# Optimization experiments

Hardware: AMD Instinct MI355X
Metric: run time of the kernel (lower is better)

The kernel has to match this reference:

```python
import jax, jax.numpy as jnp
import numpy as np

DEPTH = 2   # depth
H = 8       # heads
DH = 32     # dim_head
DIM = 256   # model dim (= H*DH)
W = 2       # sliding_window_size
C = 4       # compress_block_size == selection_block_size
NSEL = 2    # num_selected_blocks
B, S = 4, 2048


def layernorm(x, g, b, eps=1e-5):
    m = x.mean(-1, keepdims=True)
    v = jnp.var(x, axis=-1, keepdims=True)
    return (x - m) * jax.lax.rsqrt(v + eps) * g + b


def msoftmax(s, mask):
    # numerically-safe masked softmax; rows with no visible key output zeros
    s = jnp.where(mask, s, -1e9)
    p = jax.nn.softmax(s, axis=-1)
    return jnp.where(jnp.any(mask, axis=-1, keepdims=True), p, 0.0)


def nsa(x, Wq, Wk, Wv, Wg, Wo):
    # Native sparse attention: compressed + top-k selected blocks + sliding window,
    # combined with per-head sigmoid gates.
    b, s, d = x.shape
    nb = s // C
    q = (x @ Wq).reshape(b, s, H, DH).transpose(0, 2, 1, 3)  # [B,H,S,DH]
    k = (x @ Wk).reshape(b, s, H, DH).transpose(0, 2, 1, 3)
    v = (x @ Wv).reshape(b, s, H, DH).transpose(0, 2, 1, 3)
    scale = DH ** -0.5
    t = jnp.arange(s)

    # ---- compressed branch: mean-pooled KV blocks, causal over fully-past blocks
    kb = k.reshape(b, H, nb, C, DH)
    vb = v.reshape(b, H, nb, C, DH)
    kc = kb.mean(3)
    vc = vb.mean(3)
    sc = jnp.einsum('bhsd,bhnd->bhsn', q, kc) * scale       # [B,H,S,nb]
    blk_end = jnp.arange(nb) * C + (C - 1)
    cmask = blk_end[None, :] <= t[:, None]                   # [S,nb]
    pc = msoftmax(sc, cmask[None, None])
    oc = jnp.einsum('bhsn,bhnd->bhsd', pc, vc)

    # ---- selection branch: own block always + top (NSEL-1) blocks by compressed score
    own = t // C                                             # [S]
    not_own = jnp.arange(nb)[None, :] != own[:, None]        # [S,nb]
    sel_scores = jnp.where(not_own[None, None], pc, -1.0)
    top_idx = jax.lax.top_k(sel_scores, NSEL - 1)[1]         # [B,H,S,NSEL-1]
    own_idx = jnp.broadcast_to(own[None, None, :, None], (b, H, s, 1))
    idx = jnp.concatenate([own_idx, top_idx], axis=-1)       # [B,H,S,NSEL]
    idxf = idx.reshape(b, H, s * NSEL, 1, 1)
    sk = jnp.take_along_axis(kb, idxf, axis=2).reshape(b, H, s, NSEL * C, DH)
    sv = jnp.take_along_axis(vb, idxf, axis=2).reshape(b, H, s, NSEL * C, DH)
    pos = (idx[..., None] * C + jnp.arange(C)).reshape(b, H, s, NSEL * C)
    fmask = pos <= t[None, None, :, None]
    sf = jnp.einsum('bhsd,bhskd->bhsk', q, sk) * scale
    pf = msoftmax(sf, fmask)
    of = jnp.einsum('bhsk,bhskd->bhsd', pf, sv)

    # ---- sliding-window branch: causal local window of W tokens (incl. self)
    off = jnp.arange(W) - (W - 1)
    wpos = t[:, None] + off[None, :]                         # [S,W]
    widx = jnp.clip(wpos, 0, s - 1)
    kw = jnp.take(k, widx.reshape(-1), axis=2).reshape(b, H, s, W, DH)
    vw = jnp.take(v, widx.reshape(-1), axis=2).reshape(b, H, s, W, DH)
    sw = jnp.einsum('bhsd,bhsjd->bhsj', q, kw) * scale
    pw = msoftmax(sw, (wpos >= 0)[None, None])
    ow = jnp.einsum('bhsj,bhsjd->bhsd', pw, vw)

    # ---- gated combine + output projection
    g = jax.nn.sigmoid(x @ Wg).reshape(b, s, 3, H).transpose(0, 3, 1, 2)  # [B,H,S,3]
    o = g[..., 0:1] * oc + g[..., 1:2] * of + g[..., 2:3] * ow
    return o.transpose(0, 2, 1, 3).reshape(b, s, H * DH) @ Wo


def forward(x, ln_a_g, ln_a_b, Wq, Wk, Wv, Wg, Wo, ln_f_g, ln_f_b, W1, b1, W2, b2):
    for l in range(DEPTH):
        for j in range(2):  # two attention sub-layers per block
            i = l * 2 + j
            h = layernorm(x, ln_a_g[i], ln_a_b[i])
            x = x + nsa(h, Wq[i], Wk[i], Wv[i], Wg[i], Wo[i])
        h = layernorm(x, ln_f_g[l], ln_f_b[l])
        h = h @ W1[l] + b1[l]
        h = jnp.where(h > 0, h, 0.01 * h)  # LeakyReLU
        x = x + h @ W2[l] + b2[l]
    return x


def setup_inputs() -> dict:
    key = jax.random.key(0)
    ks = jax.random.split(key, 8)
    A = DEPTH * 2
    r = lambda k, shp: jax.random.normal(k, shp, jnp.float32) * 0.02
    return {
        'x': jax.random.normal(ks[0], (B, S, DIM), jnp.float32),
        'ln_a_g': jnp.ones((A, DIM), jnp.float32),
        'ln_a_b': jnp.zeros((A, DIM), jnp.float32),
        'Wq': r(ks[1], (A, DIM, H * DH)),
        'Wk': r(ks[2], (A, DIM, H * DH)),
        'Wv': r(ks[3], (A, DIM, H * DH)),
        'Wg': r(ks[4], (A, DIM, 3 * H)),
        'Wo': r(ks[5], (A, H * DH, DIM)),
        'ln_f_g': jnp.ones((DEPTH, DIM), jnp.float32),
        'ln_f_b': jnp.zeros((DEPTH, DIM), jnp.float32),
        'W1': r(ks[6], (DEPTH, DIM, 2 * DIM)),
        'b1': jnp.zeros((DEPTH, 2 * DIM), jnp.float32),
        'W2': r(ks[7], (DEPTH, 2 * DIM, DIM)),
        'b2': jnp.zeros((DEPTH, DIM), jnp.float32),
    }


def reference(x, ln_a_g, ln_a_b, Wq, Wk, Wv, Wg, Wo, ln_f_g, ln_f_b, W1, b1, W2, b2):
    return forward(x, ln_a_g, ln_a_b, Wq, Wk, Wv, Wg, Wo, ln_f_g, ln_f_b, W1, b1, W2, b2)
```

## Files before the change

kernel.cpp:

```cpp
#include <hip/hip_runtime.h>
#include <hip/hip_bf16.h>
#include <math.h>

#define NH 8
#define DH 32
#define DIM 256
#define SEQ 2048
#define BATCH 4
#define NB 512
#define QKS 512
#define VGS 320
#define SCALE 0.17677669529663687f

typedef short short8v __attribute__((ext_vector_type(8)));
typedef float float4v __attribute__((ext_vector_type(4)));

__device__ __forceinline__ float sigmoidf_(float x){ return 1.f/(1.f+__expf(-x)); }
__device__ __forceinline__ ushort f2bf(float f){
  uint b = __float_as_uint(f);
  return (ushort)((b + 0x7fffu + ((b>>16)&1u)) >> 16);
}
__device__ __forceinline__ float bf2f(ushort u){ return __uint_as_float(((uint)u)<<16); }
__device__ __forceinline__ float bflo(uint u){ return __uint_as_float(u<<16); }
__device__ __forceinline__ float bfhi(uint u){ return __uint_as_float(u & 0xffff0000u); }
__device__ __forceinline__ uint pk2(float a, float b){ return (uint)f2bf(a) | ((uint)f2bf(b)<<16); }
__device__ __forceinline__ void bfu4_to_f32(uint4 u, float* f){
  f[0]=bflo(u.x); f[1]=bfhi(u.x);
  f[2]=bflo(u.y); f[3]=bfhi(u.y);
  f[4]=bflo(u.z); f[5]=bfhi(u.z);
  f[6]=bflo(u.w); f[7]=bfhi(u.w);
}
__device__ __forceinline__ void bfu2_to_f32(uint2 u, float* f){
  f[0]=bflo(u.x); f[1]=bfhi(u.x);
  f[2]=bflo(u.y); f[3]=bfhi(u.y);
}

__global__ void copy_f32(const float* __restrict__ in, float* __restrict__ out, int n4){
  int i = blockIdx.x*blockDim.x + threadIdx.x;
  if (i < n4) ((float4*)out)[i] = ((const float4*)in)[i];
}

__global__ void build_wqk(const float* __restrict__ Wq, const float* __restrict__ Wk, float* __restrict__ out){
  int i = blockIdx.x*256 + threadIdx.x;
  if (i >= 4*256*QKS) return;
  int col = i & 511, rk = (i>>9)&255, l = i>>17;
  out[i] = (col < 256) ? Wq[((size_t)l*256+rk)*256+col] : Wk[((size_t)l*256+rk)*256+col-256];
}
__global__ void build_wvgT(const float* __restrict__ Wv, const float* __restrict__ Wg, ushort* __restrict__ out){
  int i = blockIdx.x*256 + threadIdx.x;
  if (i >= 4*VGS*256) return;
  int k = i & 255, n = (i>>8)%VGS, l = i/(VGS*256);
  float v = 0.f;
  if      (n < 256) v = Wv[((size_t)l*256+k)*256+n];
  else if (n < 280) v = Wg[((size_t)l*256+k)*24 + (n-256)];
  out[i] = f2bf(v);
}
__global__ void build_wT(const float* __restrict__ in, ushort* __restrict__ out, int L, int K, int N){
  int i = blockIdx.x*256 + threadIdx.x;
  if (i >= L*K*N) return;
  int k = i % K, n = (i/K) % N, l = i/(K*N);
  out[i] = f2bf(in[((size_t)l*K+k)*N+n]);
}

__global__ __launch_bounds__(256) void ln_k(const float* __restrict__ x, const float* __restrict__ g,
                                            const float* __restrict__ b, float* __restrict__ h,
                                            ushort* __restrict__ hb){
  int row  = blockIdx.x*4 + (threadIdx.x>>6);
  int lane = threadIdx.x & 63;
  int c = lane*4;
  const float* xr = x + (size_t)row*DIM + c;
  float4 v = *(const float4*)xr;
  float s = v.x+v.y+v.z+v.w;
  float q = v.x*v.x+v.y*v.y+v.z*v.z+v.w*v.w;
  #pragma unroll
  for (int off=32; off>0; off>>=1){ s += __shfl_xor(s, off); q += __shfl_xor(q, off); }
  float mean = s * (1.f/DIM);
  float var  = q * (1.f/DIM) - mean*mean;
  float rs = rsqrtf(var + 1e-5f);
  float4 gg = *(const float4*)(g + c);
  float4 bb = *(const float4*)(b + c);
  float4 o;
  o.x = (v.x-mean)*rs*gg.x + bb.x;
  o.y = (v.y-mean)*rs*gg.y + bb.y;
  o.z = (v.z-mean)*rs*gg.z + bb.z;
  o.w = (v.w-mean)*rs*gg.w + bb.w;
  *(float4*)(h + (size_t)row*DIM + c) = o;
  uint2 u;
  u.x = pk2(o.x, o.y);
  u.y = pk2(o.z, o.w);
  *(uint2*)&hb[(size_t)row*DIM + c] = u;
}

template<bool BIAS, bool LEAKY, bool ACC>
__global__ __launch_bounds__(256) void gemm_f32(const float* __restrict__ A, const float* __restrict__ B,
                                                const float* __restrict__ bias, float* __restrict__ C,
                                                int M, int N, int K){
  __shared__ float As[32][132];
  __shared__ float Bs[32][68];
  int tid = threadIdx.x;
  int m0 = blockIdx.x*128, n0 = blockIdx.y*64;
  int tx = tid & 15, ty = tid >> 4;
  int ar = tid >> 1;
  int ac = (tid & 1)*16;
  int bk = tid >> 3;
  int bn = (tid & 7)*8;
  const float* Ap = A + (size_t)(m0+ar)*K + ac;
  const float* Bp = B + (size_t)bk*N + n0 + bn;
  float4 apre[4], bpre[2];
  #pragma unroll
  for (int j=0;j<4;j++) apre[j] = *(const float4*)(Ap + 4*j);
  bpre[0] = *(const float4*)Bp;
  bpre[1] = *(const float4*)(Bp + 4);
  float acc[8][4];
  #pragma unroll
  for (int i=0;i<8;i++)
    #pragma unroll
    for (int j=0;j<4;j++) acc[i][j]=0.f;
  for (int k0=0; k0<K; k0+=32){
    #pragma unroll
    for (int j=0;j<4;j++){
      As[ac+4*j+0][ar]=apre[j].x; As[ac+4*j+1][ar]=apre[j].y;
      As[ac+4*j+2][ar]=apre[j].z; As[ac+4*j+3][ar]=apre[j].w;
    }
    *(float4*)&Bs[bk][bn]   = bpre[0];
    *(float4*)&Bs[bk][bn+4] = bpre[1];
    __syncthreads();
    if (k0 + 32 < K){
      #pragma unroll
      for (int j=0;j<4;j++) apre[j] = *(const float4*)(Ap + k0 + 32 + 4*j);
      bpre[0] = *(const float4*)(Bp + (size_t)(k0+32)*N);
      bpre[1] = *(const float4*)(Bp + (size_t)(k0+32)*N + 4);
    }
    #pragma unroll
    for (int kk=0;kk<32;kk++){
      float4 bv  = *(const float4*)&Bs[kk][tx*4];
      float4 av0 = *(const float4*)&As[kk][ty*8];
      float4 av1 = *(const float4*)&As[kk][ty*8+4];
      float av[8] = {av0.x,av0.y,av0.z,av0.w,av1.x,av1.y,av1.z,av1.w};
      float bw[4] = {bv.x,bv.y,bv.z,bv.w};
      #pragma unroll
      for (int i=0;i<8;i++)
        #pragma unroll
        for (int j=0;j<4;j++) acc[i][j] += av[i]*bw[j];
    }
    __syncthreads();
  }
  #pragma unroll
  for (int i=0;i<8;i++){
    int m = m0 + ty*8 + i;
    #pragma unroll
    for (int j=0;j<4;j++){
      int n = n0 + tx*4 + j;
      float val = acc[i][j];
      if (BIAS)  val += bias[n];
      if (LEAKY) val = val > 0.f ? val : 0.01f*val;
      float* cp = C + (size_t)m*N + n;
      if (ACC) val += *cp;
      *cp = val;
    }
  }
}

template<bool BIAS, bool LEAKY, bool ACC, bool OBF16>
__global__ __launch_bounds__(256) void gemm_bf16(const ushort* __restrict__ A, const ushort* __restrict__ Bt,
                                                 const float* __restrict__ bias, void* __restrict__ Cv,
                                                 int M, int N, int K){
  __shared__ ushort Al[128*64];
  __shared__ ushort Bl[64*64];
  int tid = threadIdx.x;
  int m0 = blockIdx.x*128, n0 = blockIdx.y*64;
  int w = tid>>6, lane = tid&63;
  int wm = w>>1, wn = w&1;
  float4v acc[4][2];
  #pragma unroll
  for (int i=0;i<4;i++)
    #pragma unroll
    for (int j=0;j<2;j++) acc[i][j] = (float4v){0.f,0.f,0.f,0.f};
  for (int k0=0; k0<K; k0+=64){
    #pragma unroll
    for (int i=0;i<4;i++){
      int id = tid + 256*i;
      int r = id>>3, c = id&7;
      *(uint4*)&Al[r*64 + ((c ^ (r&7))*8)] = *(const uint4*)&A[(size_t)(m0+r)*K + k0 + c*8];
    }
    #pragma unroll
    for (int i=0;i<2;i++){
      int id = tid + 256*i;
      int r = id>>3, c = id&7;
      *(uint4*)&Bl[r*64 + ((c ^ (r&7))*8)] = *(const uint4*)&Bt[(size_t)(n0+r)*K + k0 + c*8];
    }
    __syncthreads();
    #pragma unroll
    for (int kk=0; kk<2; ++kk){
      short8v a[4], bfr[2];
      #pragma unroll
      for (int mf=0; mf<4; mf++){
        int r = wm*64 + mf*16 + (lane&15);
        int c = (kk*4 + (lane>>4)) ^ (r&7);
        a[mf] = *(short8v*)&Al[r*64 + c*8];
      }
      #pragma unroll
      for (int nf=0; nf<2; nf++){
        int r = wn*32 + nf*16 + (lane&15);
        int c = (kk*4 + (lane>>4)) ^ (r&7);
        bfr[nf] = *(short8v*)&Bl[r*64 + c*8];
      }
      #pragma unroll
      for (int mf=0; mf<4; mf++)
        #pragma unroll
        for (int nf=0; nf<2; nf++)
          acc[mf][nf] = __builtin_amdgcn_mfma_f32_16x16x32_bf16(a[mf], bfr[nf], acc[mf][nf], 0, 0, 0);
    }
    __syncthreads();
  }
  #pragma unroll
  for (int nf=0; nf<2; nf++){
    int col = n0 + wn*32 + nf*16 + (lane&15);
    float bv = BIAS ? bias[col] : 0.f;
    #pragma unroll
    for (int mf=0; mf<4; mf++){
      #pragma unroll
      for (int r=0; r<4; r++){
        int row = m0 + wm*64 + mf*16 + (lane>>4)*4 + r;
        float vv = acc[mf][nf][r];
        if (BIAS) vv += bv;
        if (LEAKY) vv = vv > 0.f ? vv : 0.01f*vv;
        if (OBF16) ((ushort*)Cv)[(size_t)row*N + col] = f2bf(vv);
        else {
          float* C = (float*)Cv;
          if (ACC) vv += C[(size_t)row*N + col];
          C[(size_t)row*N + col] = vv;
        }
      }
    }
  }
}

__global__ void pool_k(const float* __restrict__ qk, const ushort* __restrict__ vg,
                       float* __restrict__ kc, ushort* __restrict__ vct){
  int i = blockIdx.x*256 + threadIdx.x;
  if (i >= BATCH*NH*NB*DH) return;
  int d = i & 31, n = (i >> 5) & 511, h = (i >> 14) & 7, b = i >> 17;
  size_t kb = ((size_t)(b*SEQ + n*4))*QKS + 256 + h*DH + d;
  kc[i] = 0.25f*(qk[kb] + qk[kb+QKS] + qk[kb+2*QKS] + qk[kb+3*QKS]);
  size_t vb = ((size_t)(b*SEQ + n*4))*VGS + h*DH + d;
  float pv = 0.25f*(bf2f(vg[vb]) + bf2f(vg[vb+VGS]) + bf2f(vg[vb+2*VGS]) + bf2f(vg[vb+3*VGS]));
  vct[(((size_t)(b*NH + h))*DH + d)*NB + n] = f2bf(pv);
}

__global__ __launch_bounds__(512, 4) void nsa_attn(
    const float* __restrict__ qk, const ushort* __restrict__ vg,
    const float* __restrict__ kc, const ushort* __restrict__ vct,
    ushort* __restrict__ o)
{
  __shared__ float  kt[64*32];
  __shared__ ushort vcT[32*72];
  __shared__ ushort Pl[64*72];
  __shared__ float4 meta[8*64];
  int e = blockIdx.x;
  int hh = e & 7;
  int b  = (e >> 3) & 3;
  int qq = (e >> 5) & 7;
  int r  = e >> 8;
  int g  = (r==0) ? (31-qq) : (r==1) ? qq : (r==2) ? (23-qq) : (8+qq);
  int tid = threadIdx.x;
  int w = tid >> 6, lane = tid & 63;
  const float*  kcg  = kc  + ((size_t)(b*NH + hh)*NB)*DH;
  const ushort* vctg = vct + ((size_t)(b*NH + hh)*DH)*NB;

  float4v acc0 = (float4v){0.f,0.f,0.f,0.f};
  float4v acc1 = (float4v){0.f,0.f,0.f,0.f};

  {
    int t = g*64 + lane;
    int own = t >> 2, nvis = (t+1) >> 2;
    int nmax = 16*(g+1);
    float qv[32];
    {
      const float4* qr = (const float4*)(qk + ((size_t)b*SEQ + t)*QKS + hh*DH);
      #pragma unroll
      for (int d8=0; d8<8; d8++){
        float4 a4 = qr[d8];
        qv[4*d8]=a4.x; qv[4*d8+1]=a4.y; qv[4*d8+2]=a4.z; qv[4*d8+3]=a4.w;
      }
    }
    float l = 0.f, best = -1e30f;
    int bn1 = -1;

    int tiles = (g + 4) >> 2;
    for (int ti=0; ti<tiles; ++ti){
      int base = ti*64;
      if (ti) __syncthreads();
      {
        const float4* sk = (const float4*)(kcg + (size_t)base*DH);
        ((float4*)kt)[tid] = sk[tid];
        if (tid < 256){
          int sd = tid >> 3, sn = (tid & 7)*8;
          *(uint4*)&vcT[sd*72 + sn] = *(const uint4*)&vctg[(size_t)sd*NB + base + sn];
        }
      }
      __syncthreads();
      int jm = nmax - base - 8*w;
      jm = jm < 0 ? 0 : (jm > 8 ? 8 : jm);
      float ps[8];
      #pragma unroll
      for (int j=0;j<8;j++) ps[j]=0.f;
      for (int j=0; j<jm; ++j){
        int rr = 8*w + j;
        int n = base + rr;
        const float4* kp = (const float4*)&kt[rr*32];
        float s = 0.f;
        #pragma unroll
        for (int d8=0; d8<8; d8++){
          float4 k4 = kp[d8];
          s += qv[4*d8]*k4.x + qv[4*d8+1]*k4.y + qv[4*d8+2]*k4.z + qv[4*d8+3]*k4.w;
        }
        s *= SCALE;
        bool act = (n < nvis);
        if (act && n != own && s > best){ best = s; bn1 = n; }
        float p = act ? __expf(s) : 0.f;
        l += p;
        ps[j] = p;
      }
      {
        uint4 u0;
        u0.x = pk2(ps[0],ps[1]);  u0.y = pk2(ps[2],ps[3]);
        u0.z = pk2(ps[4],ps[5]);  u0.w = pk2(ps[6],ps[7]);
        *(uint4*)&Pl[lane*72 + w*8] = u0;
      }
      __syncthreads();
      if (w < 4){
        #pragma unroll
        for (int ks=0; ks<2; ++ks){
          short8v bfrag = *(short8v*)&Pl [(16*w + (lane&15))*72 + ks*32 + (lane>>4)*8];
          short8v a0    = *(short8v*)&vcT[(lane&15)*72          + ks*32 + (lane>>4)*8];
          short8v a1    = *(short8v*)&vcT[((lane&15)+16)*72     + ks*32 + (lane>>4)*8];
          acc0 = __builtin_amdgcn_mfma_f32_16x16x32_bf16(a0, bfrag, acc0, 0, 0, 0);
          acc1 = __builtin_amdgcn_mfma_f32_16x16x32_bf16(a1, bfrag, acc1, 0, 0, 0);
        }
      }
    }
    meta[w*64 + lane] = make_float4(l, best, __int_as_float(bn1), 0.f);
  }
  __syncthreads();

  if (w < 4){
    int c = lane & 15, m = lane >> 4;
    int tokidx = w*16 + c;
    int t = g*64 + tokidx;
    int own = t >> 2, nvis = (t+1) >> 2;
    int dA = 4*m, dB = 16 + 4*m;
    float q8[8];
    {
      const float* qrow = qk + ((size_t)b*SEQ + t)*QKS + hh*DH;
      float4 a4 = *(const float4*)(qrow + dA);
      float4 b4 = *(const float4*)(qrow + dB);
      q8[0]=a4.x; q8[1]=a4.y; q8[2]=a4.z; q8[3]=a4.w;
      q8[4]=b4.x; q8[5]=b4.y; q8[6]=b4.z; q8[7]=b4.w;
    }
    float out8[8];
    #pragma unroll
    for (int j=0;j<4;j++){ out8[j] = acc0[j]; out8[4+j] = acc1[j]; }
    float ll = 0.f, bb = -1e30f;
    int bn = (own==0) ? 1 : 0;
    #pragma unroll
    for (int sp=0; sp<8; ++sp){
      float4 m4 = meta[sp*64 + tokidx];
      ll += m4.x;
      int mi = __float_as_int(m4.z);
      if (m4.y > bb || (m4.y == bb && mi >= 0 && mi < bn)){ bb = m4.y; bn = mi; }
    }
    const ushort* gr = vg + ((size_t)b*SEQ + t)*VGS + 256;
    float g0 = sigmoidf_(bf2f(gr[hh])), g1 = sigmoidf_(bf2f(gr[8+hh])), g2 = sigmoidf_(bf2f(gr[16+hh]));
    float inv = (nvis > 0) ? g0/ll : 0.f;
    #pragma unroll
    for (int j=0;j<8;j++) out8[j] *= inv;

    const float*  kb2 = qk + (size_t)b*SEQ*QKS + 256 + hh*DH;
    const ushort* vb2 = vg + (size_t)b*SEQ*VGS + hh*DH;
    float s2[8];
    float m2 = -1e30f;
    #pragma unroll
    for (int ki=0; ki<8; ++ki){
      int tt = (ki<4 ? own : bn)*4 + (ki&3);
      float s = -1e30f;
      if (tt <= t){
        const float* kr = kb2 + (size_t)tt*QKS;
        float4 a4 = *(const float4*)(kr + dA);
        float4 c4 = *(const float4*)(kr + dB);
        float ps = q8[0]*a4.x + q8[1]*a4.y + q8[2]*a4.z + q8[3]*a4.w
                 + q8[4]*c4.x + q8[5]*c4.y + q8[6]*c4.z + q8[7]*c4.w;
        ps += __shfl_xor(ps, 16);
        ps += __shfl_xor(ps, 32);
        s = ps*SCALE;
        m2 = fmaxf(m2, s);
      }
      s2[ki] = s;
    }
    float l2 = 0.f;
    #pragma unroll
    for (int ki=0; ki<8; ++ki)
      if (s2[ki] > -1e29f) l2 += __expf(s2[ki] - m2);
    float inv2 = g1/l2;
    #pragma unroll
    for (int ki=0; ki<8; ++ki){
      int tt = (ki<4 ? own : bn)*4 + (ki&3);
      if (tt <= t){
        float pw = __expf(s2[ki] - m2) * inv2;
        float fA[4], fB[4];
        bfu2_to_f32(*(const uint2*)(vb2 + (size_t)tt*VGS + dA), fA);
        bfu2_to_f32(*(const uint2*)(vb2 + (size_t)tt*VGS + dB), fB);
        #pragma unroll
        for (int j=0;j<4;j++){ out8[j] += pw*fA[j]; out8[4+j] += pw*fB[j]; }
      }
    }

    int tp = (t>0) ? t-1 : 0;
    float sa, sb;
    {
      const float* ka = kb2 + (size_t)tp*QKS;
      const float* kb4= kb2 + (size_t)t *QKS;
      float4 a0 = *(const float4*)(ka + dA), a1 = *(const float4*)(ka + dB);
      float4 b0 = *(const float4*)(kb4 + dA), b1 = *(const float4*)(kb4 + dB);
      float pa_ = q8[0]*a0.x + q8[1]*a0.y + q8[2]*a0.z + q8[3]*a0.w
                + q8[4]*a1.x + q8[5]*a1.y + q8[6]*a1.z + q8[7]*a1.w;
      float pb_ = q8[0]*b0.x + q8[1]*b0.y + q8[2]*b0.z + q8[3]*b0.w
                + q8[4]*b1.x + q8[5]*b1.y + q8[6]*b1.z + q8[7]*b1.w;
      pa_ += __shfl_xor(pa_, 16); pa_ += __shfl_xor(pa_, 32);
      pb_ += __shfl_xor(pb_, 16); pb_ += __shfl_xor(pb_, 32);
      sa = pa_*SCALE; sb = pb_*SCALE;
    }
    float m3 = (t>0) ? fmaxf(sa, sb) : sb;
    float pa = (t>0) ? __expf(sa-m3) : 0.f;
    float pb = __expf(sb-m3);
    float inv3 = g2/(pa+pb);
    float va[4], vaB[4], vbv[4], vbB[4];
    bfu2_to_f32(*(const uint2*)(vb2 + (size_t)tp*VGS + dA), va);
    bfu2_to_f32(*(const uint2*)(vb2 + (size_t)tp*VGS + dB), vaB);
    bfu2_to_f32(*(const uint2*)(vb2 + (size_t)t *VGS + dA), vbv);
    bfu2_to_f32(*(const uint2*)(vb2 + (size_t)t *VGS + dB), vbB);
    ushort* orow = o + ((size_t)b*SEQ + t)*DIM + hh*DH;
    float rrA[4], rrB[4];
    #pragma unroll
    for (int j=0;j<4;j++){
      rrA[j] = out8[j]   + (pa*va[j]  + pb*vbv[j])*inv3;
      rrB[j] = out8[4+j] + (pa*vaB[j] + pb*vbB[j])*inv3;
    }
    uint2 uA, uB;
    uA.x = pk2(rrA[0], rrA[1]); uA.y = pk2(rrA[2], rrA[3]);
    uB.x = pk2(rrB[0], rrB[1]); uB.y = pk2(rrB[2], rrB[3]);
    *(uint2*)&orow[dA] = uA;
    *(uint2*)&orow[dB] = uB;
  }
}

extern "C" void kernel_launch(void* const* d_in, const int* in_sizes, int n_in,
                              void* d_out, int out_size, void* d_ws, size_t ws_size,
                              hipStream_t stream) {
  const float* x_in   = (const float*)d_in[0];
  const float* ln_a_g = (const float*)d_in[1];
  const float* ln_a_b = (const float*)d_in[2];
  const float* Wq     = (const float*)d_in[3];
  const float* Wk     = (const float*)d_in[4];
  const float* Wv     = (const float*)d_in[5];
  const float* Wg     = (const float*)d_in[6];
  const float* Wo     = (const float*)d_in[7];
  const float* ln_f_g = (const float*)d_in[8];
  const float* ln_f_b = (const float*)d_in[9];
  const float* W1     = (const float*)d_in[10];
  const float* b1     = (const float*)d_in[11];
  const float* W2     = (const float*)d_in[12];
  const float* b2     = (const float*)d_in[13];

  float* xout = (float*)d_out;
  float* ws = (float*)d_ws;
  const size_t NTOK = (size_t)BATCH*SEQ;
  float* h    = ws;
  float* qkb  = h    + NTOK*DIM;
  float* kcb  = qkb  + NTOK*QKS;
  ushort* vctb = (ushort*)(kcb + (size_t)BATCH*NH*NB*DH);
  float* wqk  = (float*)(vctb + (size_t)BATCH*NH*NB*DH);
  ushort* hb   = (ushort*)(wqk + (size_t)4*DIM*QKS);
  ushort* vgu  = hb   + NTOK*DIM;
  ushort* obu  = vgu  + NTOK*VGS;
  ushort* midu = obu  + NTOK*DIM;
  ushort* wvgT = midu + NTOK*512;
  ushort* woT  = wvgT + (size_t)4*VGS*DIM;
  ushort* w1T  = woT  + (size_t)4*DIM*DIM;
  ushort* w2T  = w1T  + (size_t)2*512*DIM;

  copy_f32<<<2048, 256, 0, stream>>>(x_in, xout, (int)(NTOK*DIM/4));
  build_wqk <<<(4*256*QKS+255)/256, 256, 0, stream>>>(Wq, Wk, wqk);
  build_wvgT<<<(4*VGS*256+255)/256, 256, 0, stream>>>(Wv, Wg, wvgT);
  build_wT  <<<(4*256*256+255)/256, 256, 0, stream>>>(Wo, woT, 4, 256, 256);
  build_wT  <<<(2*256*512+255)/256, 256, 0, stream>>>(W1, w1T, 2, 256, 512);
  build_wT  <<<(2*512*256+255)/256, 256, 0, stream>>>(W2, w2T, 2, 512, 256);

  dim3 gqk(64,8), gvg(64,5), g4(64,4), g8(64,8);
  for (int i=0;i<4;i++){
    ln_k<<<2048,256,0,stream>>>(xout, ln_a_g + i*DIM, ln_a_b + i*DIM, h, hb);
    gemm_f32<false,false,false><<<gqk,256,0,stream>>>(h, wqk + (size_t)i*DIM*QKS, nullptr, qkb, 8192,QKS,256);
    gemm_bf16<false,false,false,true><<<gvg,256,0,stream>>>(hb, wvgT + (size_t)i*VGS*DIM, nullptr, vgu, 8192,VGS,256);
    pool_k<<<2048,256,0,stream>>>(qkb, vgu, kcb, vctb);
    nsa_attn<<<1024,512,0,stream>>>(qkb, vgu, kcb, vctb, obu);
    gemm_bf16<false,false,true,false><<<g4,256,0,stream>>>(obu, woT + (size_t)i*DIM*DIM, nullptr, xout, 8192,DIM,256);
    if (i & 1){
      int l = i >> 1;
      ln_k<<<2048,256,0,stream>>>(xout, ln_f_g + l*DIM, ln_f_b + l*DIM, h, hb);
      gemm_bf16<true,true,false,true><<<g8,256,0,stream>>>(hb,   w1T + (size_t)l*512*DIM, b1 + l*512, midu, 8192,512,256);
      gemm_bf16<true,false,true,false><<<g4,256,0,stream>>>(midu, w2T + (size_t)l*DIM*512, b2 + l*DIM, xout, 8192,DIM,512);
    }
  }
}
```

Measured before the change: 597.2 us.

## Process 128 queries per attention block with 4 waves for compressed-K reuse

The NSA attention kernel now handles 128 query tokens per block with 256 threads instead of 64 tokens with 512 threads. Each thread scores two queries against two compressed keys per step, and each wave issues four MFMAs per k-step, so every compressed-key tile loaded into shared memory serves twice as many queries. The aim is to cut redundant compressed-KV loads and the idle waves in the MFMA and epilogue phases. The cost is higher register pressure, fewer blocks (512), and a simpler causal load-balancing order that may leave the longest blocks unevenly spread across CUs.

```diff
diff --git a/kernel.cpp b/kernel.cpp
--- a/kernel.cpp
+++ b/kernel.cpp
@@ -24,12 +24,6 @@
 __device__ __forceinline__ float bflo(uint u){ return __uint_as_float(u<<16); }
 __device__ __forceinline__ float bfhi(uint u){ return __uint_as_float(u & 0xffff0000u); }
 __device__ __forceinline__ uint pk2(float a, float b){ return (uint)f2bf(a) | ((uint)f2bf(b)<<16); }
-__device__ __forceinline__ void bfu4_to_f32(uint4 u, float* f){
-  f[0]=bflo(u.x); f[1]=bfhi(u.x);
-  f[2]=bflo(u.y); f[3]=bfhi(u.y);
-  f[4]=bflo(u.z); f[5]=bfhi(u.z);
-  f[6]=bflo(u.w); f[7]=bfhi(u.w);
-}
 __device__ __forceinline__ void bfu2_to_f32(uint2 u, float* f){
   f[0]=bflo(u.x); f[1]=bfhi(u.x);
   f[2]=bflo(u.y); f[3]=bfhi(u.y);
@@ -248,21 +242,20 @@
   vct[(((size_t)(b*NH + h))*DH + d)*NB + n] = f2bf(pv);
 }
 
-__global__ __launch_bounds__(512, 4) void nsa_attn(
+__global__ __launch_bounds__(256, 2) void nsa_attn(
     const float* __restrict__ qk, const ushort* __restrict__ vg,
     const float* __restrict__ kc, const ushort* __restrict__ vct,
     ushort* __restrict__ o)
 {
   __shared__ float  kt[64*32];
   __shared__ ushort vcT[32*72];
-  __shared__ ushort Pl[64*72];
-  __shared__ float4 meta[8*64];
+  __shared__ ushort Pl[128*72];
+  __shared__ float4 meta[4*128];
   int e = blockIdx.x;
   int hh = e & 7;
   int b  = (e >> 3) & 3;
-  int qq = (e >> 5) & 7;
-  int r  = e >> 8;
-  int g  = (r==0) ? (31-qq) : (r==1) ? qq : (r==2) ? (23-qq) : (8+qq);
+  int gc = (e >> 5) & 7;
+  int g  = (e < 256) ? (15 - gc) : gc;
   int tid = threadIdx.x;
   int w = tid >> 6, lane = tid & 63;
   const float*  kcg  = kc  + ((size_t)(b*NH + hh)*NB)*DH;
@@ -270,187 +263,221 @@
 
   float4v acc0 = (float4v){0.f,0.f,0.f,0.f};
   float4v acc1 = (float4v){0.f,0.f,0.f,0.f};
+  float4v acc2 = (float4v){0.f,0.f,0.f,0.f};
+  float4v acc3 = (float4v){0.f,0.f,0.f,0.f};
 
   {
-    int t = g*64 + lane;
-    int own = t >> 2, nvis = (t+1) >> 2;
-    int nmax = 16*(g+1);
-    float qv[32];
+    int t0 = g*128 + lane, t1 = t0 + 64;
+    int own0 = t0 >> 2, nvis0 = (t0+1) >> 2;
+    int own1 = t1 >> 2, nvis1 = (t1+1) >> 2;
+    int nmax = 32*(g+1);
+    float qv0[32], qv1[32];
     {
-      const float4* qr = (const float4*)(qk + ((size_t)b*SEQ + t)*QKS + hh*DH);
+      const float4* q0 = (const float4*)(qk + ((size_t)b*SEQ + t0)*QKS + hh*DH);
+      const float4* q1 = (const float4*)(qk + ((size_t)b*SEQ + t1)*QKS + hh*DH);
       #pragma unroll
       for (int d8=0; d8<8; d8++){
-        float4 a4 = qr[d8];
-        qv[4*d8]=a4.x; qv[4*d8+1]=a4.y; qv[4*d8+2]=a4.z; qv[4*d8+3]=a4.w;
-      }
-    }
-    float l = 0.f, best = -1e30f;
-    int bn1 = -1;
-
-    int tiles = (g + 4) >> 2;
+        float4 a4 = q0[d8]; float4 b4 = q1[d8];
+        qv0[4*d8]=a4.x; qv0[4*d8+1]=a4.y; qv0[4*d8+2]=a4.z; qv0[4*d8+3]=a4.w;
+        qv1[4*d8]=b4.x; qv1[4*d8+1]=b4.y; qv1[4*d8+2]=b4.z; qv1[4*d8+3]=b4.w;
+      }
+    }
+    float l0 = 0.f, l1 = 0.f, best0 = -1e30f, best1 = -1e30f;
+    int ibn0 = -1, ibn1 = -1;
+
+    int tiles = (g + 2) >> 1;
     for (int ti=0; ti<tiles; ++ti){
       int base = ti*64;
       if (ti) __syncthreads();
       {
         const float4* sk = (const float4*)(kcg + (size_t)base*DH);
-        ((float4*)kt)[tid] = sk[tid];
-        if (tid < 256){
-          int sd = tid >> 3, sn = (tid & 7)*8;
-          *(uint4*)&vcT[sd*72 + sn] = *(const uint4*)&vctg[(size_t)sd*NB + base + sn];
-        }
+        ((float4*)kt)[tid]     = sk[tid];
+        ((float4*)kt)[tid+256] = sk[tid+256];
+        int sd = tid >> 3, sn = (tid & 7)*8;
+        *(uint4*)&vcT[sd*72 + sn] = *(const uint4*)&vctg[(size_t)sd*NB + base + sn];
       }
       __syncthreads();
-      int jm = nmax - base - 8*w;
-      jm = jm < 0 ? 0 : (jm > 8 ? 8 : jm);
-      float ps[8];
-      #pragma unroll
-      for (int j=0;j<8;j++) ps[j]=0.f;
-      for (int j=0; j<jm; ++j){
-        int rr = 8*w + j;
-        int n = base + rr;
-        const float4* kp = (const float4*)&kt[rr*32];
-        float s = 0.f;
+      int jm = nmax - base - 16*w;
+      jm = jm < 0 ? 0 : (jm > 16 ? 16 : jm);
+      uint psu0[8], psu1[8];
+      #pragma unroll
+      for (int j=0;j<8;j++){ psu0[j]=0u; psu1[j]=0u; }
+      for (int j=0; j<jm; j+=2){
+        int rr0 = 16*w + j, rr1 = rr0 + 1;
+        int n0 = base + rr0, n1 = base + rr1;
+        bool row1ok = (j+1 < jm);
+        const float4* kp0 = (const float4*)&kt[rr0*32];
+        const float4* kp1 = (const float4*)&kt[rr1*32];
+        float s00=0.f, s10=0.f, s01=0.f, s11=0.f;
         #pragma unroll
         for (int d8=0; d8<8; d8++){
-          float4 k4 = kp[d8];
-          s += qv[4*d8]*k4.x + qv[4*d8+1]*k4.y + qv[4*d8+2]*k4.z + qv[4*d8+3]*k4.w;
+          float4 k4a = kp0[d8];
+          float4 k4b = kp1[d8];
+          s00 += qv0[4*d8]*k4a.x + qv0[4*d8+1]*k4a.y + qv0[4*d8+2]*k4a.z + qv0[4*d8+3]*k4a.w;
+          s10 += qv1[4*d8]*k4a.x + qv1[4*d8+1]*k4a.y + qv1[4*d8+2]*k4a.z + qv1[4*d8+3]*k4a.w;
+          s01 += qv0[4*d8]*k4b.x + qv0[4*d8+1]*k4b.y + qv0[4*d8+2]*k4b.z + qv0[4*d8+3]*k4b.w;
+          s11 += qv1[4*d8]*k4b.x + qv1[4*d8+1]*k4b.y + qv1[4*d8+2]*k4b.z + qv1[4*d8+3]*k4b.w;
         }
-        s *= SCALE;
-        bool act = (n < nvis);
-        if (act && n != own && s > best){ best = s; bn1 = n; }
-        float p = act ? __expf(s) : 0.f;
-        l += p;
-        ps[j] = p;
+        s00 *= SCALE; s10 *= SCALE; s01 *= SCALE; s11 *= SCALE;
+        bool a00 = (n0 < nvis0), a10 = (n0 < nvis1);
+        if (a00 && n0 != own0 && s00 > best0){ best0 = s00; ibn0 = n0; }
+        if (a10 && n0 != own1 && s10 > best1){ best1 = s10; ibn1 = n0; }
+        float p00 = a00 ? __expf(s00) : 0.f;
+        float p10 = a10 ? __expf(s10) : 0.f;
+        float p01 = 0.f, p11 = 0.f;
+        if (row1ok){
+          bool a01 = (n1 < nvis0), a11 = (n1 < nvis1);
+          if (a01 && n1 != own0 && s01 > best0){ best0 = s01; ibn0 = n1; }
+          if (a11 && n1 != own1 && s11 > best1){ best1 = s11; ibn1 = n1; }
+          p01 = a01 ? __expf(s01) : 0.f;
+          p11 = a11 ? __expf(s11) : 0.f;
+        }
+        l0 += p00 + p01;
+        l1 += p10 + p11;
+        psu0[j>>1] = pk2(p00, p01);
+        psu1[j>>1] = pk2(p10, p11);
       }
       {
-        uint4 u0;
-        u0.x = pk2(ps[0],ps[1]);  u0.y = pk2(ps[2],ps[3]);
-        u0.z = pk2(ps[4],ps[5]);  u0.w = pk2(ps[6],ps[7]);
-        *(uint4*)&Pl[lane*72 + w*8] = u0;
+        uint4 u0 = make_uint4(psu0[0],psu0[1],psu0[2],psu0[3]);
+        uint4 u1 = make_uint4(psu0[4],psu0[5],psu0[6],psu0[7]);
+        uint4 u2 = make_uint4(psu1[0],psu1[1],psu1[2],psu1[3]);
+        uint4 u3 = make_uint4(psu1[4],psu1[5],psu1[6],psu1[7]);
+        *(uint4*)&Pl[lane*72 + w*16]           = u0;
+        *(uint4*)&Pl[lane*72 + w*16 + 8]       = u1;
+        *(uint4*)&Pl[(64+lane)*72 + w*16]      = u2;
+        *(uint4*)&Pl[(64+lane)*72 + w*16 + 8]  = u3;
       }
       __syncthreads();
-      if (w < 4){
-        #pragma unroll
-        for (int ks=0; ks<2; ++ks){
-          short8v bfrag = *(short8v*)&Pl [(16*w + (lane&15))*72 + ks*32 + (lane>>4)*8];
-          short8v a0    = *(short8v*)&vcT[(lane&15)*72          + ks*32 + (lane>>4)*8];
-          short8v a1    = *(short8v*)&vcT[((lane&15)+16)*72     + ks*32 + (lane>>4)*8];
-          acc0 = __builtin_amdgcn_mfma_f32_16x16x32_bf16(a0, bfrag, acc0, 0, 0, 0);
-          acc1 = __builtin_amdgcn_mfma_f32_16x16x32_bf16(a1, bfrag, acc1, 0, 0, 0);
-        }
-      }
-    }
-    meta[w*64 + lane] = make_float4(l, best, __int_as_float(bn1), 0.f);
+      #pragma unroll
+      for (int ks=0; ks<2; ++ks){
+        short8v bf0 = *(short8v*)&Pl [(16*w + (lane&15))*72      + ks*32 + (lane>>4)*8];
+        short8v bf1 = *(short8v*)&Pl [(64 + 16*w + (lane&15))*72 + ks*32 + (lane>>4)*8];
+        short8v a0  = *(short8v*)&vcT[(lane&15)*72               + ks*32 + (lane>>4)*8];
+        short8v a1  = *(short8v*)&vcT[((lane&15)+16)*72          + ks*32 + (lane>>4)*8];
+        acc0 = __builtin_amdgcn_mfma_f32_16x16x32_bf16(a0, bf0, acc0, 0, 0, 0);
+        acc1 = __builtin_amdgcn_mfma_f32_16x16x32_bf16(a1, bf0, acc1, 0, 0, 0);
+        acc2 = __builtin_amdgcn_mfma_f32_16x16x32_bf16(a0, bf1, acc2, 0, 0, 0);
+        acc3 = __builtin_amdgcn_mfma_f32_16x16x32_bf16(a1, bf1, acc3, 0, 0, 0);
+      }
+    }
+    meta[w*128 + lane]      = make_float4(l0, best0, __int_as_float(ibn0), 0.f);
+    meta[w*128 + 64 + lane] = make_float4(l1, best1, __int_as_float(ibn1), 0.f);
   }
   __syncthreads();
 
-  if (w < 4){
+  {
     int c = lane & 15, m = lane >> 4;
-    int tokidx = w*16 + c;
-    int t = g*64 + tokidx;
-    int own = t >> 2, nvis = (t+1) >> 2;
     int dA = 4*m, dB = 16 + 4*m;
-    float q8[8];
-    {
-      const float* qrow = qk + ((size_t)b*SEQ + t)*QKS + hh*DH;
-      float4 a4 = *(const float4*)(qrow + dA);
-      float4 b4 = *(const float4*)(qrow + dB);
-      q8[0]=a4.x; q8[1]=a4.y; q8[2]=a4.z; q8[3]=a4.w;
-      q8[4]=b4.x; q8[5]=b4.y; q8[6]=b4.z; q8[7]=b4.w;
-    }
-    float out8[8];
-    #pragma unroll
-    for (int j=0;j<4;j++){ out8[j] = acc0[j]; out8[4+j] = acc1[j]; }
-    float ll = 0.f, bb = -1e30f;
-    int bn = (own==0) ? 1 : 0;
-    #pragma unroll
-    for (int sp=0; sp<8; ++sp){
-      float4 m4 = meta[sp*64 + tokidx];
-      ll += m4.x;
-      int mi = __float_as_int(m4.z);
-      if (m4.y > bb || (m4.y == bb && mi >= 0 && mi < bn)){ bb = m4.y; bn = mi; }
-    }
-    const ushort* gr = vg + ((size_t)b*SEQ + t)*VGS + 256;
-    float g0 = sigmoidf_(bf2f(gr[hh])), g1 = sigmoidf_(bf2f(gr[8+hh])), g2 = sigmoidf_(bf2f(gr[16+hh]));
-    float inv = (nvis > 0) ? g0/ll : 0.f;
-    #pragma unroll
-    for (int j=0;j<8;j++) out8[j] *= inv;
-
     const float*  kb2 = qk + (size_t)b*SEQ*QKS + 256 + hh*DH;
     const ushort* vb2 = vg + (size_t)b*SEQ*VGS + hh*DH;
-    float s2[8];
-    float m2 = -1e30f;
-    #pragma unroll
-    for (int ki=0; ki<8; ++ki){
-      int tt = (ki<4 ? own : bn)*4 + (ki&3);
-      float s = -1e30f;
-      if (tt <= t){
-        const float* kr = kb2 + (size_t)tt*QKS;
-        float4 a4 = *(const float4*)(kr + dA);
-        float4 c4 = *(const float4*)(kr + dB);
-        float ps = q8[0]*a4.x + q8[1]*a4.y + q8[2]*a4.z + q8[3]*a4.w
-                 + q8[4]*c4.x + q8[5]*c4.y + q8[6]*c4.z + q8[7]*c4.w;
-        ps += __shfl_xor(ps, 16);
-        ps += __shfl_xor(ps, 32);
-        s = ps*SCALE;
-        m2 = fmaxf(m2, s);
-      }
-      s2[ki] = s;
-    }
-    float l2 = 0.f;
-    #pragma unroll
-    for (int ki=0; ki<8; ++ki)
-      if (s2[ki] > -1e29f) l2 += __expf(s2[ki] - m2);
-    float inv2 = g1/l2;
-    #pragma unroll
-    for (int ki=0; ki<8; ++ki){
-      int tt = (ki<4 ? own : bn)*4 + (ki&3);
-      if (tt <= t){
-        float pw = __expf(s2[ki] - m2) * inv2;
-        float fA[4], fB[4];
-        bfu2_to_f32(*(const uint2*)(vb2 + (size_t)tt*VGS + dA), fA);
-        bfu2_to_f32(*(const uint2*)(vb2 + (size_t)tt*VGS + dB), fB);
-        #pragma unroll
-        for (int j=0;j<4;j++){ out8[j] += pw*fA[j]; out8[4+j] += pw*fB[j]; }
-      }
-    }
-
-    int tp = (t>0) ? t-1 : 0;
-    float sa, sb;
-    {
-      const float* ka = kb2 + (size_t)tp*QKS;
-      const float* kb4= kb2 + (size_t)t *QKS;
-      float4 a0 = *(const float4*)(ka + dA), a1 = *(const float4*)(ka + dB);
-      float4 b0 = *(const float4*)(kb4 + dA), b1 = *(const float4*)(kb4 + dB);
-      float pa_ = q8[0]*a0.x + q8[1]*a0.y + q8[2]*a0.z + q8[3]*a0.w
-                + q8[4]*a1.x + q8[5]*a1.y + q8[6]*a1.z + q8[7]*a1.w;
-      float pb_ = q8[0]*b0.x + q8[1]*b0.y + q8[2]*b0.z + q8[3]*b0.w
-                + q8[4]*b1.x + q8[5]*b1.y + q8[6]*b1.z + q8[7]*b1.w;
-      pa_ += __shfl_xor(pa_, 16); pa_ += __shfl_xor(pa_, 32);
-      pb_ += __shfl_xor(pb_, 16); pb_ += __shfl_xor(pb_, 32);
-      sa = pa_*SCALE; sb = pb_*SCALE;
-    }
-    float m3 = (t>0) ? fmaxf(sa, sb) : sb;
-    float pa = (t>0) ? __expf(sa-m3) : 0.f;
-    float pb = __expf(sb-m3);
-    float inv3 = g2/(pa+pb);
-    float va[4], vaB[4], vbv[4], vbB[4];
-    bfu2_to_f32(*(const uint2*)(vb2 + (size_t)tp*VGS + dA), va);
-    bfu2_to_f32(*(const uint2*)(vb2 + (size_t)tp*VGS + dB), vaB);
-    bfu2_to_f32(*(const uint2*)(vb2 + (size_t)t *VGS + dA), vbv);
-    bfu2_to_f32(*(const uint2*)(vb2 + (size_t)t *VGS + dB), vbB);
-    ushort* orow = o + ((size_t)b*SEQ + t)*DIM + hh*DH;
-    float rrA[4], rrB[4];
-    #pragma unroll
-    for (int j=0;j<4;j++){
-      rrA[j] = out8[j]   + (pa*va[j]  + pb*vbv[j])*inv3;
-      rrB[j] = out8[4+j] + (pa*vaB[j] + pb*vbB[j])*inv3;
-    }
-    uint2 uA, uB;
-    uA.x = pk2(rrA[0], rrA[1]); uA.y = pk2(rrA[2], rrA[3]);
-    uB.x = pk2(rrB[0], rrB[1]); uB.y = pk2(rrB[2], rrB[3]);
-    *(uint2*)&orow[dA] = uA;
-    *(uint2*)&orow[dB] = uB;
+    #pragma unroll
+    for (int which=0; which<2; ++which){
+      int tokidx = which*64 + w*16 + c;
+      int t = g*128 + tokidx;
+      int own = t >> 2, nvis = (t+1) >> 2;
+      float q8[8];
+      {
+        const float* qrow = qk + ((size_t)b*SEQ + t)*QKS + hh*DH;
+        float4 a4 = *(const float4*)(qrow + dA);
+        float4 b4 = *(const float4*)(qrow + dB);
+        q8[0]=a4.x; q8[1]=a4.y; q8[2]=a4.z; q8[3]=a4.w;
+        q8[4]=b4.x; q8[5]=b4.y; q8[6]=b4.z; q8[7]=b4.w;
+      }
+      float out8[8];
+      #pragma unroll
+      for (int j=0;j<4;j++){
+        out8[j]   = which ? acc2[j] : acc0[j];
+        out8[4+j] = which ? acc3[j] : acc1[j];
+      }
+      float ll = 0.f, bb = -1e30f;
+      int bn = (own==0) ? 1 : 0;
+      #pragma unroll
+      for (int sp=0; sp<4; ++sp){
+        float4 m4 = meta[sp*128 + tokidx];
+        ll += m4.x;
+        int mi = __float_as_int(m4.z);
+        if (m4.y > bb || (m4.y == bb && mi >= 0 && mi < bn)){ bb = m4.y; bn = mi; }
+      }
+      const ushort* gr = vg + ((size_t)b*SEQ + t)*VGS + 256;
+      float g0 = sigmoidf_(bf2f(gr[hh])), g1 = sigmoidf_(bf2f(gr[8+hh])), g2 = sigmoidf_(bf2f(gr[16+hh]));
+      float inv = (nvis > 0) ? g0/ll : 0.f;
+      #pragma unroll
+      for (int j=0;j<8;j++) out8[j] *= inv;
+
+      float s2[8];
+      float m2 = -1e30f;
+      #pragma unroll
+      for (int ki=0; ki<8; ++ki){
+        int tt = (ki<4 ? own : bn)*4 + (ki&3);
+        float s = -1e30f;
+        if (tt <= t){
+          const float* kr = kb2 + (size_t)tt*QKS;
+          float4 a4 = *(const float4*)(kr + dA);
+          float4 c4 = *(const float4*)(kr + dB);
+          float ps = q8[0]*a4.x + q8[1]*a4.y + q8[2]*a4.z + q8[3]*a4.w
+                   + q8[4]*c4.x + q8[5]*c4.y + q8[6]*c4.z + q8[7]*c4.w;
+          ps += __shfl_xor(ps, 16);
+          ps += __shfl_xor(ps, 32);
+          s = ps*SCALE;
+          m2 = fmaxf(m2, s);
+        }
+        s2[ki] = s;
+      }
+      float l2 = 0.f;
+      #pragma unroll
+      for (int ki=0; ki<8; ++ki)
+        if (s2[ki] > -1e29f) l2 += __expf(s2[ki] - m2);
+      float inv2 = g1/l2;
+      #pragma unroll
+      for (int ki=0; ki<8; ++ki){
+        int tt = (ki<4 ? own : bn)*4 + (ki&3);
+        if (tt <= t){
+          float pw = __expf(s2[ki] - m2) * inv2;
+          float fA[4], fB[4];
+          bfu2_to_f32(*(const uint2*)(vb2 + (size_t)tt*VGS + dA), fA);
+          bfu2_to_f32(*(const uint2*)(vb2 + (size_t)tt*VGS + dB), fB);
+          #pragma unroll
+          for (int j=0;j<4;j++){ out8[j] += pw*fA[j]; out8[4+j] += pw*fB[j]; }
+        }
+      }
+
+      int tp = (t>0) ? t-1 : 0;
+      float sa, sb;
+      {
+        const float* ka = kb2 + (size_t)tp*QKS;
+        const float* kb4= kb2 + (size_t)t *QKS;
+        float4 a0 = *(const float4*)(ka + dA), a1 = *(const float4*)(ka + dB);
+        float4 b0 = *(const float4*)(kb4 + dA), b1 = *(const float4*)(kb4 + dB);
+        float pa_ = q8[0]*a0.x + q8[1]*a0.y + q8[2]*a0.z + q8[3]*a0.w
+                  + q8[4]*a1.x + q8[5]*a1.y + q8[6]*a1.z + q8[7]*a1.w;
+        float pb_ = q8[0]*b0.x + q8[1]*b0.y + q8[2]*b0.z + q8[3]*b0.w
+                  + q8[4]*b1.x + q8[5]*b1.y + q8[6]*b1.z + q8[7]*b1.w;
+        pa_ += __shfl_xor(pa_, 16); pa_ += __shfl_xor(pa_, 32);
+        pb_ += __shfl_xor(pb_, 16); pb_ += __shfl_xor(pb_, 32);
+        sa = pa_*SCALE; sb = pb_*SCALE;
+      }
+      float m3 = (t>0) ? fmaxf(sa, sb) : sb;
+      float pa = (t>0) ? __expf(sa-m3) : 0.f;
+      float pb = __expf(sb-m3);
+      float inv3 = g2/(pa+pb);
+      float va[4], vaB[4], vbv[4], vbB[4];
+      bfu2_to_f32(*(const uint2*)(vb2 + (size_t)tp*VGS + dA), va);
+      bfu2_to_f32(*(const uint2*)(vb2 + (size_t)tp*VGS + dB), vaB);
+      bfu2_to_f32(*(const uint2*)(vb2 + (size_t)t *VGS + dA), vbv);
+      bfu2_to_f32(*(const uint2*)(vb2 + (size_t)t *VGS + dB), vbB);
+      ushort* orow = o + ((size_t)b*SEQ + t)*DIM + hh*DH;
+      float rrA[4], rrB[4];
+      #pragma unroll
+      for (int j=0;j<4;j++){
+        rrA[j] = out8[j]   + (pa*va[j]  + pb*vbv[j])*inv3;
+        rrB[j] = out8[4+j] + (pa*vaB[j] + pb*vbB[j])*inv3;
+      }
+      uint2 uA, uB;
+      uA.x = pk2(rrA[0], rrA[1]); uA.y = pk2(rrA[2], rrA[3]);
+      uB.x = pk2(rrB[0], rrB[1]); uB.y = pk2(rrB[2], rrB[3]);
+      *(uint2*)&orow[dA] = uA;
+      *(uint2*)&orow[dB] = uB;
+    }
   }
 }
 
@@ -502,7 +529,7 @@
     gemm_f32<false,false,false><<<gqk,256,0,stream>>>(h, wqk + (size_t)i*DIM*QKS, nullptr, qkb, 8192,QKS,256);
     gemm_bf16<false,false,false,true><<<gvg,256,0,stream>>>(hb, wvgT + (size_t)i*VGS*DIM, nullptr, vgu, 8192,VGS,256);
     pool_k<<<2048,256,0,stream>>>(qkb, vgu, kcb, vctb);
-    nsa_attn<<<1024,512,0,stream>>>(qkb, vgu, kcb, vctb, obu);
+    nsa_attn<<<512,256,0,stream>>>(qkb, vgu, kcb, vctb, obu);
     gemm_bf16<false,false,true,false><<<g4,256,0,stream>>>(obu, woT + (size_t)i*DIM*DIM, nullptr, xout, 8192,DIM,256);
     if (i & 1){
       int l = i >> 1;
```

Measured after the change: 591.7 us. Within noise of the previous version (-0.9%).
